# Optimization experiments

Measured on AMD Instinct MI355X. Metric: run time of the kernel, lower is better.

Reference implementation:

```python
import jax, jax.numpy as jnp
import numpy as np

K = 8
LOCAL_WINDOW_RATIO = 0.25
NEG = -1e9
LN_EPS = 1e-5
NORM_EPS = 1e-12


def _window_indices(H, W):
    lws = max(3, int(min(H, W) * LOCAL_WINDOW_RATIO))
    if lws % 2 == 0:
        lws += 1
    half = lws // 2
    off = jnp.arange(-half, half + 1)
    dy, dx = jnp.meshgrid(off, off, indexing='ij')          # [lws,lws]
    dy = dy.reshape(-1); dx = dx.reshape(-1)                 # [w2]
    py, px = jnp.meshgrid(jnp.arange(H), jnp.arange(W), indexing='ij')
    py = py.reshape(-1); px = px.reshape(-1)                 # [HW]
    ny = py[:, None] + dy[None, :]                           # [HW,w2]
    nx = px[:, None] + dx[None, :]
    valid = (ny >= 0) & (ny < H) & (nx >= 0) & (nx < W)
    idx = jnp.clip(ny, 0, H - 1) * W + jnp.clip(nx, 0, W - 1)
    return idx, valid


def setup_inputs() -> dict:
    key = jax.random.key(0)
    ks = jax.random.split(key, 5)
    B, C, H, W = 4, 96, 48, 48
    return {
        'x': jax.random.normal(ks[0], (B, C, H, W), jnp.float32),
        'w1': jax.random.normal(ks[1], (2 * C, C), jnp.float32) * 0.05,
        'b1': jax.random.normal(ks[2], (2 * C,), jnp.float32) * 0.05,
        'w2': jax.random.normal(ks[3], (C, 2 * C), jnp.float32) * 0.05,
        'b2': jax.random.normal(ks[4], (C,), jnp.float32) * 0.05,
        'ln_w': jnp.ones((C,), jnp.float32),
        'ln_b': jnp.zeros((C,), jnp.float32),
    }


def reference(x, w1, b1, w2, b2, ln_w, ln_b):
    B, C, H, W = x.shape
    HW = H * W
    idx_w, valid = _window_indices(H, W)                     # [HW,w2]

    x_flat = x.transpose(0, 2, 3, 1).reshape(B, HW, C)       # [B,HW,C]
    n = jnp.linalg.norm(x_flat, axis=-1, keepdims=True)
    x_n = x_flat / jnp.maximum(n, NORM_EPS)

    win_n = x_n[:, idx_w, :]                                 # [B,HW,w2,C]
    sims = jnp.einsum('bpc,bpwc->bpw', x_n, win_n)           # cosine sim
    sims = jnp.where(valid[None], sims, NEG)

    # every pixel has >= (half+1)^2 >= K valid neighbors, so top-k stays valid
    top_sim, top_idx = jax.lax.top_k(sims, K)                # [B,HW,K]
    wts = jax.nn.softmax(top_sim, axis=-1)                   # exp/sum over top-k

    idx_g = jnp.take_along_axis(jnp.broadcast_to(idx_w[None], sims.shape), top_idx, axis=-1)  # [B,HW,K]
    feats = x_flat[jnp.arange(B)[:, None, None], idx_g]      # [B,HW,K,C] (un-normalized)
    agg = jnp.einsum('bpk,bpkc->bpc', wts, feats)            # [B,HW,C]

    mu = jnp.mean(x_flat, axis=-1, keepdims=True)
    var = jnp.var(x_flat, axis=-1, keepdims=True)
    x_ln = (x_flat - mu) / jnp.sqrt(var + LN_EPS) * ln_w + ln_b

    enhanced = agg + x_ln                                    # [B,HW,C]
    h = jax.nn.relu(jnp.einsum('bpc,dc->bpd', enhanced, w1) + b1)
    ffn = jnp.einsum('bpd,cd->bpc', h, w2) + b2
    out = enhanced + ffn
    return out.reshape(B, H, W, C).transpose(0, 3, 1, 2)
```

## Files before the change

### kernel.cpp

```cpp
#include <hip/hip_runtime.h>
#include <math.h>

#define BATCH 4
#define CH    96
#define HH    48
#define WW    48
#define HWPIX (HH*WW)
#define NPIX  (BATCH*HWPIX)
#define WIN   13
#define WIN2  169
#define HALF  6
#define TOPK  8
#define NEGV  (-1000000000.0f)

__global__ __launch_bounds__(256) void k0_wq(
    const float* __restrict__ w1, const float* __restrict__ w2,
    float4* __restrict__ w1Q, float4* __restrict__ w2Q)
{
    int i = blockIdx.x * 256 + threadIdx.x;
    if (i < 4608) {
        int c4 = i / 192, j = i % 192;
        w1Q[c4 * 192 + j] = *(const float4*)(w1 + j * 96 + c4 * 4);
    } else {
        int k = i - 4608;
        int j4 = k / 96, c = k % 96;
        w2Q[j4 * 96 + c] = *(const float4*)(w2 + c * 192 + j4 * 4);
    }
}

__global__ __launch_bounds__(256) void k1_prep(
    const float* __restrict__ x, float* __restrict__ xt2,
    float* __restrict__ invn, float* __restrict__ muv, float* __restrict__ rsd)
{
    __shared__ float lds[96][17];
    int bid = blockIdx.x;
    int b   = bid / 144;
    int p0  = (bid % 144) * 16;
    int t   = threadIdx.x;

    #pragma unroll
    for (int it = 0; it < 6; ++it) {
        int e = t + it * 256;
        int c = e >> 4;
        int p = e & 15;
        lds[c][p] = x[(b * CH + c) * HWPIX + p0 + p];
    }
    __syncthreads();

    if (t < 16) {
        float s = 0.f, ss = 0.f;
        #pragma unroll
        for (int c = 0; c < CH; ++c) { float v = lds[c][t]; s += v; ss += v * v; }
        int gpix = b * HWPIX + p0 + t;
        invn[gpix] = 1.0f / fmaxf(sqrtf(ss), 1e-12f);
        float m = s * (1.0f / 96.0f);
        muv[gpix] = m;
        rsd[gpix] = rsqrtf(ss * (1.0f / 96.0f) - m * m + 1e-5f);
    }

    float4* x4 = (float4*)xt2;
    for (int i = t; i < 384; i += 256) {
        int p = i & 15;
        int s = i >> 4;
        float4 v = make_float4(lds[4*s][p], lds[4*s+1][p],
                               lds[4*s+2][p], lds[4*s+3][p]);
        x4[s * NPIX + b * HWPIX + p0 + p] = v;
    }
}

__global__ __launch_bounds__(256) void k2_knn(
    const float* __restrict__ xt2, const float* __restrict__ invn,
    const float* __restrict__ muv, const float* __restrict__ rsd,
    const float* __restrict__ lnw, const float* __restrict__ lnb,
    float* __restrict__ enh)
{
    __shared__ float own[4][96];
    int t    = threadIdx.x;
    int wv   = t >> 6;
    int lane = t & 63;
    int gp   = blockIdx.x * 4 + wv;
    int b    = gp / HWPIX;
    int p    = gp - b * HWPIX;
    int py   = p / WW;
    int px   = p - py * WW;
    const float4* x4 = (const float4*)xt2;

    float4 ownv = make_float4(0.f, 0.f, 0.f, 0.f);
    if (lane < 24) {
        ownv = x4[lane * NPIX + gp];
        ((float4*)(own[wv]))[lane] = ownv;
    }
    float inp = invn[gp];
    float mu  = muv[gp];
    float rs  = rsd[gp];

    float v0 = -2e9f, v1 = -2e9f, v2 = -2e9f;
    const float4* ov = (const float4*)(own[wv]);
    #pragma unroll
    for (int k = 0; k < 3; ++k) {
        int n = lane + 64 * k;
        float sim = -2e9f;
        if (n < WIN2) {
            int dy = n / WIN - HALF;
            int dx = n - (dy + HALF) * WIN - HALF;
            int ny = py + dy, nx = px + dx;
            if (ny >= 0 && ny < HH && nx >= 0 && nx < WW) {
                int q = b * HWPIX + ny * WW + nx;
                float inq = invn[q];
                const float4* rp = x4 + q;
                float ax = 0.f, ay = 0.f, az = 0.f, aw = 0.f;
                #pragma unroll
                for (int s = 0; s < 24; ++s) {
                    float4 a  = ov[s];
                    float4 bb = rp[s * NPIX];
                    ax += a.x * bb.x; ay += a.y * bb.y;
                    az += a.z * bb.z; aw += a.w * bb.w;
                }
                sim = ((ax + ay) + (az + aw)) * inp * inq;
            } else {
                sim = NEGV;
            }
        }
        if (k == 0) v0 = sim; else if (k == 1) v1 = sim; else v2 = sim;
    }

    float tv[TOPK]; int tn[TOPK];
    #pragma unroll
    for (int r = 0; r < TOPK; ++r) {
        float m = fmaxf(fmaxf(v0, v1), v2);
        #pragma unroll
        for (int off = 1; off < 64; off <<= 1)
            m = fmaxf(m, __shfl_xor(m, off));
        unsigned long long m0 = __ballot(v0 == m);
        unsigned long long m1 = __ballot(v1 == m);
        unsigned long long m2 = __ballot(v2 == m);
        int n;
        if (m0)      n = (int)__builtin_ctzll(m0);
        else if (m1) n = 64 + (int)__builtin_ctzll(m1);
        else         n = 128 + (int)__builtin_ctzll(m2);
        tv[r] = m; tn[r] = n;
        int kk = n >> 6, ll = n & 63;
        if (ll == lane) {
            if (kk == 0)      v0 = -2e9f;
            else if (kk == 1) v1 = -2e9f;
            else              v2 = -2e9f;
        }
    }

    float wts[TOPK]; int qn[TOPK];
    float wsum = 0.f;
    #pragma unroll
    for (int r = 0; r < TOPK; ++r) {
        float e = expf(tv[r] - tv[0]);
        wts[r] = e; wsum += e;
        int n  = tn[r];
        int dy = n / WIN - HALF;
        int dx = n - (dy + HALF) * WIN - HALF;
        int gy = min(max(py + dy, 0), HH - 1);
        int gx = min(max(px + dx, 0), WW - 1);
        qn[r]  = b * HWPIX + gy * WW + gx;
    }
    float winv = 1.0f / wsum;

    if (lane < 24) {
        const float4* base = x4 + lane * NPIX;
        float4 g = make_float4(0.f, 0.f, 0.f, 0.f);
        #pragma unroll
        for (int r = 0; r < TOPK; ++r) {
            float4 f = base[qn[r]];
            float w = wts[r];
            g.x += w * f.x; g.y += w * f.y;
            g.z += w * f.z; g.w += w * f.w;
        }
        float4 lw = ((const float4*)lnw)[lane];
        float4 lb = ((const float4*)lnb)[lane];
        float4 e;
        e.x = g.x * winv + (ownv.x - mu) * rs * lw.x + lb.x;
        e.y = g.y * winv + (ownv.y - mu) * rs * lw.y + lb.y;
        e.z = g.z * winv + (ownv.z - mu) * rs * lw.z + lb.z;
        e.w = g.w * winv + (ownv.w - mu) * rs * lw.w + lb.w;
        ((float4*)(enh + gp * CH))[lane] = e;
    }
}

__global__ __launch_bounds__(192) void k3_ffn(
    const float* __restrict__ enh, const float4* __restrict__ w1Q,
    const float* __restrict__ b1, const float4* __restrict__ w2Q,
    const float* __restrict__ b2, float* __restrict__ out)
{
    __shared__ float hl[8][200];
    int g  = blockIdx.x;
    int b  = g / 288;
    int p0 = (g % 288) * 8;
    int t  = threadIdx.x;
    const float4* ebase = (const float4*)(enh + (b * HWPIX + p0) * CH);

    {
        int j = t;
        float a0=0.f,a1=0.f,a2=0.f,a3=0.f,a4=0.f,a5=0.f,a6=0.f,a7=0.f;
        #pragma unroll 4
        for (int c4 = 0; c4 < 24; ++c4) {
            float4 w = w1Q[c4 * 192 + j];
            float4 v0 = ebase[0*24 + c4];
            float4 v1 = ebase[1*24 + c4];
            float4 v2 = ebase[2*24 + c4];
            float4 v3 = ebase[3*24 + c4];
            float4 v4 = ebase[4*24 + c4];
            float4 v5 = ebase[5*24 + c4];
            float4 v6 = ebase[6*24 + c4];
            float4 v7 = ebase[7*24 + c4];
            a0 += v0.x*w.x + v0.y*w.y + v0.z*w.z + v0.w*w.w;
            a1 += v1.x*w.x + v1.y*w.y + v1.z*w.z + v1.w*w.w;
            a2 += v2.x*w.x + v2.y*w.y + v2.z*w.z + v2.w*w.w;
            a3 += v3.x*w.x + v3.y*w.y + v3.z*w.z + v3.w*w.w;
            a4 += v4.x*w.x + v4.y*w.y + v4.z*w.z + v4.w*w.w;
            a5 += v5.x*w.x + v5.y*w.y + v5.z*w.z + v5.w*w.w;
            a6 += v6.x*w.x + v6.y*w.y + v6.z*w.z + v6.w*w.w;
            a7 += v7.x*w.x + v7.y*w.y + v7.z*w.z + v7.w*w.w;
        }
        float bj = b1[j];
        hl[0][j] = fmaxf(a0 + bj, 0.f);
        hl[1][j] = fmaxf(a1 + bj, 0.f);
        hl[2][j] = fmaxf(a2 + bj, 0.f);
        hl[3][j] = fmaxf(a3 + bj, 0.f);
        hl[4][j] = fmaxf(a4 + bj, 0.f);
        hl[5][j] = fmaxf(a5 + bj, 0.f);
        hl[6][j] = fmaxf(a6 + bj, 0.f);
        hl[7][j] = fmaxf(a7 + bj, 0.f);
    }
    __syncthreads();

    {
        int c    = (t >= 96) ? t - 96 : t;
        int half = (t >= 96) ? 1 : 0;
        int q0p  = half * 4;
        const float4* h0 = (const float4*)(&hl[q0p    ][0]);
        const float4* h1 = (const float4*)(&hl[q0p + 1][0]);
        const float4* h2 = (const float4*)(&hl[q0p + 2][0]);
        const float4* h3 = (const float4*)(&hl[q0p + 3][0]);
        float s0 = 0.f, s1 = 0.f, s2 = 0.f, s3 = 0.f;
        #pragma unroll 6
        for (int j4 = 0; j4 < 48; ++j4) {
            float4 w = w2Q[j4 * 96 + c];
            float4 u0 = h0[j4], u1 = h1[j4], u2 = h2[j4], u3 = h3[j4];
            s0 += u0.x*w.x + u0.y*w.y + u0.z*w.z + u0.w*w.w;
            s1 += u1.x*w.x + u1.y*w.y + u1.z*w.z + u1.w*w.w;
            s2 += u2.x*w.x + u2.y*w.y + u2.z*w.z + u2.w*w.w;
            s3 += u3.x*w.x + u3.y*w.y + u3.z*w.z + u3.w*w.w;
        }
        float bc = b2[c];
        int pb = p0 + q0p;
        out[(b * CH + c) * HWPIX + pb + 0] =
            enh[(b * HWPIX + pb + 0) * CH + c] + s0 + bc;
        out[(b * CH + c) * HWPIX + pb + 1] =
            enh[(b * HWPIX + pb + 1) * CH + c] + s1 + bc;
        out[(b * CH + c) * HWPIX + pb + 2] =
            enh[(b * HWPIX + pb + 2) * CH + c] + s2 + bc;
        out[(b * CH + c) * HWPIX + pb + 3] =
            enh[(b * HWPIX + pb + 3) * CH + c] + s3 + bc;
    }
}

extern "C" void kernel_launch(void* const* d_in, const int* in_sizes, int n_in,
                              void* d_out, int out_size, void* d_ws, size_t ws_size,
                              hipStream_t stream)
{
    const float* x   = (const float*)d_in[0];
    const float* w1  = (const float*)d_in[1];
    const float* b1  = (const float*)d_in[2];
    const float* w2  = (const float*)d_in[3];
    const float* b2  = (const float*)d_in[4];
    const float* lnw = (const float*)d_in[5];
    const float* lnb = (const float*)d_in[6];
    float* out = (float*)d_out;

    float* xt2 = out;

    float* ws   = (float*)d_ws;
    float* enh  = ws;
    float* invn = enh + NPIX * CH;
    float* muv  = invn + NPIX;
    float* rsd  = muv + NPIX;
    float* w1Qf = rsd + NPIX;
    float* w2Qf = w1Qf + 192 * 96;

    hipLaunchKernelGGL(k0_wq, dim3(36), dim3(256), 0, stream,
                       w1, w2, (float4*)w1Qf, (float4*)w2Qf);
    hipLaunchKernelGGL(k1_prep, dim3(576), dim3(256), 0, stream,
                       x, xt2, invn, muv, rsd);
    hipLaunchKernelGGL(k2_knn, dim3(NPIX / 4), dim3(256), 0, stream,
                       xt2, invn, muv, rsd, lnw, lnb, enh);
    hipLaunchKernelGGL(k3_ffn, dim3(1152), dim3(192), 0, stream,
                       enh, (const float4*)w1Qf, b1, (const float4*)w2Qf, b2, out);
}
```

Measured before the change: 74.48 us.

## Split FFN into hidden and output kernels with channel-chunked layouts

The fused per-8-pixel FFN kernel is replaced by two kernels. The first computes the ReLU hidden activations into a workspace buffer in a channel-chunked float4 layout. The second computes the output projection plus residual and writes NCHW output directly. The KNN kernel now stores enhanced features in a chunked SoA layout so the FFN kernels get coalesced per-pixel loads and more parallelism. The cost is an extra launch and a round trip of the hidden activations through global memory, and the new path only runs when the workspace is large enough.

New measurement: 104.7 us. 40.6% more time.

```diff
diff --git a/kernel.cpp b/kernel.cpp
--- a/kernel.cpp
+++ b/kernel.cpp
@@ -68,6 +68,7 @@
     }
 }
 
+template <bool CHUNK_ENH>
 __global__ __launch_bounds__(256) void k2_knn(
     const float* __restrict__ xt2, const float* __restrict__ invn,
     const float* __restrict__ muv, const float* __restrict__ rsd,
@@ -179,8 +180,82 @@
         e.y = g.y * winv + (ownv.y - mu) * rs * lw.y + lb.y;
         e.z = g.z * winv + (ownv.z - mu) * rs * lw.z + lb.z;
         e.w = g.w * winv + (ownv.w - mu) * rs * lw.w + lb.w;
-        ((float4*)(enh + gp * CH))[lane] = e;
-    }
+        if (CHUNK_ENH)
+            ((float4*)enh)[lane * NPIX + gp] = e;
+        else
+            ((float4*)(enh + gp * CH))[lane] = e;
+    }
+}
+
+__global__ __launch_bounds__(256) void k3a_h(
+    const float* __restrict__ enh2, const float4* __restrict__ w1Q,
+    const float* __restrict__ b1, float4* __restrict__ hbuf2)
+{
+    int bid = blockIdx.x;
+    int jq  = bid / 144;
+    int pg  = bid % 144;
+    int t   = threadIdx.x;
+    int pix = t & 63;
+    int wv  = t >> 6;
+    int j0  = jq * 16 + wv * 4;
+    int gp  = pg * 64 + pix;
+    const float4* e4p = (const float4*)enh2;
+
+    float a0 = 0.f, a1 = 0.f, a2 = 0.f, a3 = 0.f;
+    #pragma unroll
+    for (int c4 = 0; c4 < 24; ++c4) {
+        float4 e  = e4p[c4 * NPIX + gp];
+        float4 wA = w1Q[c4 * 192 + j0    ];
+        float4 wB = w1Q[c4 * 192 + j0 + 1];
+        float4 wC = w1Q[c4 * 192 + j0 + 2];
+        float4 wD = w1Q[c4 * 192 + j0 + 3];
+        a0 += e.x*wA.x + e.y*wA.y + e.z*wA.z + e.w*wA.w;
+        a1 += e.x*wB.x + e.y*wB.y + e.z*wB.z + e.w*wB.w;
+        a2 += e.x*wC.x + e.y*wC.y + e.z*wC.z + e.w*wC.w;
+        a3 += e.x*wD.x + e.y*wD.y + e.z*wD.z + e.w*wD.w;
+    }
+    float4 h;
+    h.x = fmaxf(a0 + b1[j0    ], 0.f);
+    h.y = fmaxf(a1 + b1[j0 + 1], 0.f);
+    h.z = fmaxf(a2 + b1[j0 + 2], 0.f);
+    h.w = fmaxf(a3 + b1[j0 + 3], 0.f);
+    hbuf2[(j0 >> 2) * NPIX + gp] = h;
+}
+
+__global__ __launch_bounds__(256) void k3b_out(
+    const float* __restrict__ enh2, const float4* __restrict__ hbuf2,
+    const float4* __restrict__ w2Q, const float* __restrict__ b2,
+    float* __restrict__ out)
+{
+    int bid = blockIdx.x;
+    int cq  = bid / 144;
+    int pg  = bid % 144;
+    int t   = threadIdx.x;
+    int pix = t & 63;
+    int wv  = t >> 6;
+    int c0  = cq * 16 + wv * 4;
+    int gp  = pg * 64 + pix;
+
+    float s0 = 0.f, s1 = 0.f, s2 = 0.f, s3 = 0.f;
+    #pragma unroll 8
+    for (int j4 = 0; j4 < 48; ++j4) {
+        float4 h  = hbuf2[j4 * NPIX + gp];
+        float4 wA = w2Q[j4 * 96 + c0    ];
+        float4 wB = w2Q[j4 * 96 + c0 + 1];
+        float4 wC = w2Q[j4 * 96 + c0 + 2];
+        float4 wD = w2Q[j4 * 96 + c0 + 3];
+        s0 += h.x*wA.x + h.y*wA.y + h.z*wA.z + h.w*wA.w;
+        s1 += h.x*wB.x + h.y*wB.y + h.z*wB.z + h.w*wB.w;
+        s2 += h.x*wC.x + h.y*wC.y + h.z*wC.z + h.w*wC.w;
+        s3 += h.x*wD.x + h.y*wD.y + h.z*wD.z + h.w*wD.w;
+    }
+    float4 er = ((const float4*)enh2)[(c0 >> 2) * NPIX + gp];
+    int b = gp / HWPIX;
+    int p = gp - b * HWPIX;
+    out[(b * CH + c0    ) * HWPIX + p] = er.x + s0 + b2[c0    ];
+    out[(b * CH + c0 + 1) * HWPIX + p] = er.y + s1 + b2[c0 + 1];
+    out[(b * CH + c0 + 2) * HWPIX + p] = er.z + s2 + b2[c0 + 2];
+    out[(b * CH + c0 + 3) * HWPIX + p] = er.w + s3 + b2[c0 + 3];
 }
 
 __global__ __launch_bounds__(192) void k3_ffn(
@@ -283,13 +358,25 @@
     float* rsd  = muv + NPIX;
     float* w1Qf = rsd + NPIX;
     float* w2Qf = w1Qf + 192 * 96;
+    float* hbuf = w2Qf + 192 * 96;
+
+    bool split = ws_size >= (size_t)2718720 * sizeof(float);
 
     hipLaunchKernelGGL(k0_wq, dim3(36), dim3(256), 0, stream,
                        w1, w2, (float4*)w1Qf, (float4*)w2Qf);
     hipLaunchKernelGGL(k1_prep, dim3(576), dim3(256), 0, stream,
                        x, xt2, invn, muv, rsd);
-    hipLaunchKernelGGL(k2_knn, dim3(NPIX / 4), dim3(256), 0, stream,
-                       xt2, invn, muv, rsd, lnw, lnb, enh);
-    hipLaunchKernelGGL(k3_ffn, dim3(1152), dim3(192), 0, stream,
-                       enh, (const float4*)w1Qf, b1, (const float4*)w2Qf, b2, out);
-}
+    if (split) {
+        hipLaunchKernelGGL(k2_knn<true>, dim3(NPIX / 4), dim3(256), 0, stream,
+                           xt2, invn, muv, rsd, lnw, lnb, enh);
+        hipLaunchKernelGGL(k3a_h, dim3(1728), dim3(256), 0, stream,
+                           enh, (const float4*)w1Qf, b1, (float4*)hbuf);
+        hipLaunchKernelGGL(k3b_out, dim3(864), dim3(256), 0, stream,
+                           enh, (const float4*)hbuf, (const float4*)w2Qf, b2, out);
+    } else {
+        hipLaunchKernelGGL(k2_knn<false>, dim3(NPIX / 4), dim3(256), 0, stream,
+                           xt2, invn, muv, rsd, lnw, lnb, enh);
+        hipLaunchKernelGGL(k3_ffn, dim3(1152), dim3(192), 0, stream,
+                           enh, (const float4*)w1Qf, b1, (const float4*)w2Qf, b2, out);
+    }
+}
```
